# Performance work log

Hardware: AMD Instinct MI355X
Metric: run time of the kernel (lower is better)

The kernel has to match this reference:

```python
import jax, jax.numpy as jnp
import numpy as np

COEFF = 0.97  # de-emphasis coefficient (module init kwarg)


def setup_inputs() -> dict:
    key = jax.random.key(0)
    waveform = jax.random.normal(key, (32, 2, 480000), dtype=jnp.float32)
    return {"waveform": waveform}


def reference(waveform) -> jnp.ndarray:
    # y[n] = x[n] + COEFF * y[n-1] along the last axis.
    # Expressed as a first-order linear recurrence y_n = a_n*y_{n-1} + b_n
    # with a_n = COEFF (constant), b_n = x[n], solved with a log-depth
    # associative scan: (a1,b1) o (a2,b2) = (a1*a2, a2*b1 + b2).
    a = jnp.full_like(waveform, COEFF)

    def combine(left, right):
        a_l, b_l = left
        a_r, b_r = right
        return (a_l * a_r, a_r * b_l + b_r)

    _, y = jax.lax.associative_scan(combine, (a, waveform), axis=-1)
    return y
```

## Files before the change

kernel.cpp:

```cpp
#include <hip/hip_runtime.h>


#define COEFF 0.97f
#define ROW_LEN 480000
#define SEG 4
#define SPAN_W 256
#define HALO 512
#define P_HALO 2
#define P_OUT 15
#define P_TOT (P_OUT + P_HALO)
#define OUT_W (P_OUT * SPAN_W)
#define WPR (ROW_LEN / OUT_W)
#define BLOCK 256
#define WAVES (BLOCK / 64)
#define PF 8

typedef float v4f __attribute__((ext_vector_type(4)));

constexpr float fpow(float b, int n) {
    float r = 1.0f;
    for (int i = 0; i < n; ++i) r *= b;
    return r;
}
constexpr float S0 = fpow(COEFF, 4);
constexpr float S1 = fpow(COEFF, 8);
constexpr float S2 = fpow(COEFF, 16);
constexpr float S3 = fpow(COEFF, 32);
constexpr float S4 = fpow(COEFF, 64);
constexpr float S5 = fpow(COEFF, 128);
constexpr float CP = fpow(COEFF, SPAN_W);
constexpr float C1P = fpow(COEFF, 1);
constexpr float C2P = fpow(COEFF, 2);
constexpr float C3P = fpow(COEFF, 3);
constexpr float C4P = fpow(COEFF, 4);

__global__ __launch_bounds__(BLOCK, 8) void deemph_kernel(const float* __restrict__ x,
                                                          float* __restrict__ y) {
    const int lane = threadIdx.x & 63;
    const int wave = threadIdx.x >> 6;
    const int widx = blockIdx.x * WAVES + wave;
    if (widx >= WPR) return;
    const int row  = blockIdx.y;

    const float* __restrict__ xrow = x + (long long)row * ROW_LEN;
    float* __restrict__ yrow       = y + (long long)row * ROW_LEN;

    const int lbase = widx * OUT_W - HALO + 4 * lane;

    float Aex = 1.0f;
    if (lane & 1)  Aex *= S0;
    if (lane & 2)  Aex *= S1;
    if (lane & 4)  Aex *= S2;
    if (lane & 8)  Aex *= S3;
    if (lane & 16) Aex *= S4;
    if (lane & 32) Aex *= S5;

    v4f rb[PF];
    #pragma unroll
    for (int q = 0; q < PF; ++q) {
        const int e = lbase + q * SPAN_W;
        v4f v = {0.0f, 0.0f, 0.0f, 0.0f};
        if (e >= 0 && e < ROW_LEN) v = *(const v4f*)(xrow + e);
        rb[q] = v;
    }

    float c = 0.0f;
    #pragma unroll
    for (int p = 0; p < P_TOT; ++p) {
        v4f v = rb[p % PF];
        if (p + PF < P_TOT) {
            const int e2 = lbase + (p + PF) * SPAN_W;
            v4f nv = {0.0f, 0.0f, 0.0f, 0.0f};
            if (e2 >= 0 && e2 < ROW_LEN) nv = *(const v4f*)(xrow + e2);
            rb[p % PF] = nv;
        }

        const float l0 = v.x;
        const float l1 = fmaf(COEFF, l0, v.y);
        const float l2 = fmaf(COEFF, l1, v.z);
        const float l3 = fmaf(COEFF, l2, v.w);

        float Bv = l3, Bp;
        Bp = __shfl_up(Bv, 1);  if (lane >= 1)  Bv = fmaf(S0, Bp, Bv);
        Bp = __shfl_up(Bv, 2);  if (lane >= 2)  Bv = fmaf(S1, Bp, Bv);
        Bp = __shfl_up(Bv, 4);  if (lane >= 4)  Bv = fmaf(S2, Bp, Bv);
        Bp = __shfl_up(Bv, 8);  if (lane >= 8)  Bv = fmaf(S3, Bp, Bv);
        Bp = __shfl_up(Bv, 16); if (lane >= 16) Bv = fmaf(S4, Bp, Bv);
        Bp = __shfl_up(Bv, 32); if (lane >= 32) Bv = fmaf(S5, Bp, Bv);
        float Bex = __shfl_up(Bv, 1);
        if (lane == 0) Bex = 0.0f;
        const float B63 = __shfl(Bv, 63);

        const float Kt = fmaf(c, Aex, Bex);
        c = fmaf(c, CP, B63);

        if (p >= P_HALO) {
            const int e = lbase + p * SPAN_W;
            if (e < ROW_LEN) {
                v4f o;
                o.x = fmaf(Kt, C1P, l0);
                o.y = fmaf(Kt, C2P, l1);
                o.z = fmaf(Kt, C3P, l2);
                o.w = fmaf(Kt, C4P, l3);
                __builtin_nontemporal_store(o, (v4f*)(yrow + e));
            }
        }
    }
}

extern "C" void kernel_launch(void* const* d_in, const int* in_sizes, int n_in,
                              void* d_out, int out_size, void* d_ws, size_t ws_size,
                              hipStream_t stream) {
    (void)n_in; (void)d_ws; (void)ws_size; (void)out_size;
    const float* x = (const float*)d_in[0];
    float* y = (float*)d_out;
    const int n_rows = in_sizes[0] / ROW_LEN;
    dim3 grid((WPR + WAVES - 1) / WAVES, n_rows);
    deemph_kernel<<<grid, BLOCK, 0, stream>>>(x, y);
}
```

Measured before the change: 218.4 us.

## Batch all spans' loads and interleave shuffle scans across spans

All seventeen per-lane vector loads are issued up front, and the wave-level shuffle scan runs on all spans at once, so the seventeen independent shuffle chains interleave instead of running one dependent chain per span. The grid is flattened to 1D so waves pack across row boundaries, the halo-boundary checks are replaced by clamping with an explicit carry reset on the first window, and the broadcast of lane 63 uses readlane. Nontemporal stores become plain stores. Register pressure rises sharply, so launch bounds are relaxed to 4 blocks per SM, which may cost occupancy.

Measured after the change: 220.2 us. About the same (+0.8%).

```diff
diff --git a/kernel.cpp b/kernel.cpp
--- a/kernel.cpp
+++ b/kernel.cpp
@@ -3,7 +3,6 @@
 
 #define COEFF 0.97f
 #define ROW_LEN 480000
-#define SEG 4
 #define SPAN_W 256
 #define HALO 512
 #define P_HALO 2
@@ -13,7 +12,6 @@
 #define WPR (ROW_LEN / OUT_W)
 #define BLOCK 256
 #define WAVES (BLOCK / 64)
-#define PF 8
 
 typedef float v4f __attribute__((ext_vector_type(4)));
 
@@ -34,13 +32,29 @@
 constexpr float C3P = fpow(COEFF, 3);
 constexpr float C4P = fpow(COEFF, 4);
 
-__global__ __launch_bounds__(BLOCK, 8) void deemph_kernel(const float* __restrict__ x,
-                                                          float* __restrict__ y) {
+__device__ __forceinline__ float bcast63(float v) {
+    return __int_as_float(__builtin_amdgcn_readlane(__float_as_int(v), 63));
+}
+
+template <int D>
+__device__ __forceinline__ void scan_step(float (&Bv)[P_TOT], float F, int lane) {
+    float Bp[P_TOT];
+    #pragma unroll
+    for (int t = 0; t < P_TOT; ++t) Bp[t] = __shfl_up(Bv[t], D);
+    #pragma unroll
+    for (int t = 0; t < P_TOT; ++t)
+        if (lane >= D) Bv[t] = fmaf(F, Bp[t], Bv[t]);
+}
+
+__global__ __launch_bounds__(BLOCK, 4) void deemph_kernel(const float* __restrict__ x,
+                                                          float* __restrict__ y,
+                                                          int n_rows) {
     const int lane = threadIdx.x & 63;
     const int wave = threadIdx.x >> 6;
-    const int widx = blockIdx.x * WAVES + wave;
-    if (widx >= WPR) return;
-    const int row  = blockIdx.y;
+    const int gw   = blockIdx.x * WAVES + wave;
+    const int row  = gw / WPR;
+    const int widx = gw - row * WPR;
+    if (row >= n_rows) return;
 
     const float* __restrict__ xrow = x + (long long)row * ROW_LEN;
     float* __restrict__ yrow       = y + (long long)row * ROW_LEN;
@@ -55,55 +69,56 @@
     if (lane & 16) Aex *= S4;
     if (lane & 32) Aex *= S5;
 
-    v4f rb[PF];
+    v4f rb[P_TOT];
     #pragma unroll
-    for (int q = 0; q < PF; ++q) {
-        const int e = lbase + q * SPAN_W;
-        v4f v = {0.0f, 0.0f, 0.0f, 0.0f};
-        if (e >= 0 && e < ROW_LEN) v = *(const v4f*)(xrow + e);
-        rb[q] = v;
+    for (int t = 0; t < P_TOT; ++t) {
+        int e = lbase + t * SPAN_W;
+        e = e < 0 ? 0 : e;
+        rb[t] = *(const v4f*)(xrow + e);
     }
+    asm volatile("" ::: "memory");
+
+    #pragma unroll
+    for (int t = 0; t < P_TOT; ++t) {
+        rb[t].y = fmaf(COEFF, rb[t].x, rb[t].y);
+        rb[t].z = fmaf(COEFF, rb[t].y, rb[t].z);
+        rb[t].w = fmaf(COEFF, rb[t].z, rb[t].w);
+    }
+
+    float Bv[P_TOT];
+    #pragma unroll
+    for (int t = 0; t < P_TOT; ++t) Bv[t] = rb[t].w;
+    scan_step<1>(Bv, S0, lane);
+    scan_step<2>(Bv, S1, lane);
+    scan_step<4>(Bv, S2, lane);
+    scan_step<8>(Bv, S3, lane);
+    scan_step<16>(Bv, S4, lane);
+    scan_step<32>(Bv, S5, lane);
+
+    float Bex[P_TOT];
+    #pragma unroll
+    for (int t = 0; t < P_TOT; ++t) {
+        Bex[t] = __shfl_up(Bv[t], 1);
+        if (lane == 0) Bex[t] = 0.0f;
+    }
+    float B63[P_TOT];
+    #pragma unroll
+    for (int t = 0; t < P_TOT; ++t) B63[t] = bcast63(Bv[t]);
 
     float c = 0.0f;
     #pragma unroll
-    for (int p = 0; p < P_TOT; ++p) {
-        v4f v = rb[p % PF];
-        if (p + PF < P_TOT) {
-            const int e2 = lbase + (p + PF) * SPAN_W;
-            v4f nv = {0.0f, 0.0f, 0.0f, 0.0f};
-            if (e2 >= 0 && e2 < ROW_LEN) nv = *(const v4f*)(xrow + e2);
-            rb[p % PF] = nv;
-        }
-
-        const float l0 = v.x;
-        const float l1 = fmaf(COEFF, l0, v.y);
-        const float l2 = fmaf(COEFF, l1, v.z);
-        const float l3 = fmaf(COEFF, l2, v.w);
-
-        float Bv = l3, Bp;
-        Bp = __shfl_up(Bv, 1);  if (lane >= 1)  Bv = fmaf(S0, Bp, Bv);
-        Bp = __shfl_up(Bv, 2);  if (lane >= 2)  Bv = fmaf(S1, Bp, Bv);
-        Bp = __shfl_up(Bv, 4);  if (lane >= 4)  Bv = fmaf(S2, Bp, Bv);
-        Bp = __shfl_up(Bv, 8);  if (lane >= 8)  Bv = fmaf(S3, Bp, Bv);
-        Bp = __shfl_up(Bv, 16); if (lane >= 16) Bv = fmaf(S4, Bp, Bv);
-        Bp = __shfl_up(Bv, 32); if (lane >= 32) Bv = fmaf(S5, Bp, Bv);
-        float Bex = __shfl_up(Bv, 1);
-        if (lane == 0) Bex = 0.0f;
-        const float B63 = __shfl(Bv, 63);
-
-        const float Kt = fmaf(c, Aex, Bex);
-        c = fmaf(c, CP, B63);
-
-        if (p >= P_HALO) {
-            const int e = lbase + p * SPAN_W;
-            if (e < ROW_LEN) {
-                v4f o;
-                o.x = fmaf(Kt, C1P, l0);
-                o.y = fmaf(Kt, C2P, l1);
-                o.z = fmaf(Kt, C3P, l2);
-                o.w = fmaf(Kt, C4P, l3);
-                __builtin_nontemporal_store(o, (v4f*)(yrow + e));
-            }
+    for (int t = 0; t < P_TOT; ++t) {
+        if (t == P_HALO) c = (widx == 0) ? 0.0f : c;
+        const float Kt = fmaf(c, Aex, Bex[t]);
+        c = fmaf(c, CP, B63[t]);
+        if (t >= P_HALO) {
+            const int e = lbase + t * SPAN_W;
+            v4f o;
+            o.x = fmaf(Kt, C1P, rb[t].x);
+            o.y = fmaf(Kt, C2P, rb[t].y);
+            o.z = fmaf(Kt, C3P, rb[t].z);
+            o.w = fmaf(Kt, C4P, rb[t].w);
+            *(v4f*)(yrow + e) = o;
         }
     }
 }
@@ -115,6 +130,6 @@
     const float* x = (const float*)d_in[0];
     float* y = (float*)d_out;
     const int n_rows = in_sizes[0] / ROW_LEN;
-    dim3 grid((WPR + WAVES - 1) / WAVES, n_rows);
-    deemph_kernel<<<grid, BLOCK, 0, stream>>>(x, y);
+    const int nblocks = (WPR * n_rows + WAVES - 1) / WAVES;
+    deemph_kernel<<<dim3(nblocks), BLOCK, 0, stream>>>(x, y, n_rows);
 }
```

## Stream input through LDS with async global_load_lds ring and flattened grid

Applied to the files above, without the earlier changes.

Replaces the register prefetch buffer with a per-wave 6-slot LDS ring filled by global_load_lds DMA, with explicit vmcnt waits computed at compile time per pass. It also flattens the 2D grid into a 1D wave index so no waves sit idle at row ends, computes the exclusive prefix algebraically instead of with an extra shuffle, and uses readlane for the broadcast. Stores become normal rather than nontemporal, and bounds checks are dropped by clamping the halo address and zeroing the carry at row start. The goal is to cut VGPR pressure and load latency for a memory-bound scan, at the cost of fragile hand-counted waitcnt ordering and LDS usage per block.

Result: no change. 219.0 us (+0.3%).

```diff
diff --git a/kernel.cpp b/kernel.cpp
--- a/kernel.cpp
+++ b/kernel.cpp
@@ -3,7 +3,6 @@
 
 #define COEFF 0.97f
 #define ROW_LEN 480000
-#define SEG 4
 #define SPAN_W 256
 #define HALO 512
 #define P_HALO 2
@@ -13,7 +12,7 @@
 #define WPR (ROW_LEN / OUT_W)
 #define BLOCK 256
 #define WAVES (BLOCK / 64)
-#define PF 8
+#define RING 6
 
 typedef float v4f __attribute__((ext_vector_type(4)));
 
@@ -28,24 +27,107 @@
 constexpr float S3 = fpow(COEFF, 32);
 constexpr float S4 = fpow(COEFF, 64);
 constexpr float S5 = fpow(COEFF, 128);
-constexpr float CP = fpow(COEFF, SPAN_W);
+constexpr float CP  = fpow(COEFF, SPAN_W);
 constexpr float C1P = fpow(COEFF, 1);
 constexpr float C2P = fpow(COEFF, 2);
 constexpr float C3P = fpow(COEFF, 3);
 constexpr float C4P = fpow(COEFF, 4);
+constexpr float IC4 = 1.0f / fpow(COEFF, 4);
 
-__global__ __launch_bounds__(BLOCK, 8) void deemph_kernel(const float* __restrict__ x,
-                                                          float* __restrict__ y) {
+constexpr int wcnt(int P) {
+    const int hi  = (P + RING - 1 < P_TOT - 1) ? P + RING - 1 : P_TOT - 1;
+    const int dma = hi - P;
+    const int lo  = (P - RING > P_HALO) ? P - RING : P_HALO;
+    int st = P - lo;
+    if (st < 0) st = 0;
+    return dma + st;
+}
+
+__device__ __forceinline__ float bcast63(float v) {
+    return __int_as_float(__builtin_amdgcn_readlane(__float_as_int(v), 63));
+}
+
+__device__ __forceinline__ void issue_dma(const float* src, v4f* slot) {
+    __builtin_amdgcn_global_load_lds(
+        (const __attribute__((address_space(1))) void*)src,
+        (__attribute__((address_space(3))) void*)slot, 16, 0, 0);
+}
+
+struct WaveCtx {
+    const float* xrow;
+    float* yrow;
+    int   base0;
+    int   lane;
+    float Aex;
+    bool  row_start;
+};
+
+template <int P>
+__device__ __forceinline__ void run_pass(const WaveCtx& cx, v4f (*slots)[64],
+                                         float& c) {
+    if constexpr (P < P_TOT) {
+        asm volatile("s_waitcnt vmcnt(%0)" :: "i"(wcnt(P)) : "memory");
+
+        v4f v = slots[P % RING][cx.lane];
+        asm volatile("s_waitcnt lgkmcnt(0)" ::: "memory");
+
+        if constexpr (P + RING < P_TOT) {
+            const int be = cx.base0 + (P + RING) * SPAN_W;
+            issue_dma(cx.xrow + be + 4 * cx.lane, &slots[P % RING][0]);
+        }
+
+        const float l0 = v.x;
+        const float l1 = fmaf(COEFF, l0, v.y);
+        const float l2 = fmaf(COEFF, l1, v.z);
+        const float l3 = fmaf(COEFF, l2, v.w);
+
+        float Bv = l3, Bp;
+        Bp = __shfl_up(Bv, 1);  if (cx.lane >= 1)  Bv = fmaf(S0, Bp, Bv);
+        Bp = __shfl_up(Bv, 2);  if (cx.lane >= 2)  Bv = fmaf(S1, Bp, Bv);
+        Bp = __shfl_up(Bv, 4);  if (cx.lane >= 4)  Bv = fmaf(S2, Bp, Bv);
+        Bp = __shfl_up(Bv, 8);  if (cx.lane >= 8)  Bv = fmaf(S3, Bp, Bv);
+        Bp = __shfl_up(Bv, 16); if (cx.lane >= 16) Bv = fmaf(S4, Bp, Bv);
+        Bp = __shfl_up(Bv, 32); if (cx.lane >= 32) Bv = fmaf(S5, Bp, Bv);
+
+        const float Bex = (Bv - l3) * IC4;
+        const float B63 = bcast63(Bv);
+
+        float cc = c;
+        if constexpr (P == P_HALO) { if (cx.row_start) cc = 0.0f; }
+        const float Kt = fmaf(cc, cx.Aex, Bex);
+        c = fmaf(cc, CP, B63);
+
+        if constexpr (P >= P_HALO) {
+            const int e = cx.base0 + P * SPAN_W + 4 * cx.lane;
+            v4f o;
+            o.x = fmaf(Kt, C1P, l0);
+            o.y = fmaf(Kt, C2P, l1);
+            o.z = fmaf(Kt, C3P, l2);
+            o.w = fmaf(Kt, C4P, l3);
+            *(v4f*)(cx.yrow + e) = o;
+        }
+
+        run_pass<P + 1>(cx, slots, c);
+    }
+}
+
+__global__ __launch_bounds__(BLOCK, 6) void deemph_kernel(const float* __restrict__ x,
+                                                          float* __restrict__ y,
+                                                          int n_rows) {
+    __shared__ v4f lds[WAVES][RING][64];
     const int lane = threadIdx.x & 63;
     const int wave = threadIdx.x >> 6;
-    const int widx = blockIdx.x * WAVES + wave;
-    if (widx >= WPR) return;
-    const int row  = blockIdx.y;
+    const int gw   = blockIdx.x * WAVES + wave;
+    const int row  = gw / WPR;
+    const int widx = gw - row * WPR;
+    if (row >= n_rows) return;
 
-    const float* __restrict__ xrow = x + (long long)row * ROW_LEN;
-    float* __restrict__ yrow       = y + (long long)row * ROW_LEN;
-
-    const int lbase = widx * OUT_W - HALO + 4 * lane;
+    WaveCtx cx;
+    cx.xrow  = x + (long long)row * ROW_LEN;
+    cx.yrow  = y + (long long)row * ROW_LEN;
+    cx.base0 = widx * OUT_W - HALO;
+    cx.lane  = lane;
+    cx.row_start = (widx == 0);
 
     float Aex = 1.0f;
     if (lane & 1)  Aex *= S0;
@@ -54,58 +136,17 @@
     if (lane & 8)  Aex *= S3;
     if (lane & 16) Aex *= S4;
     if (lane & 32) Aex *= S5;
+    cx.Aex = Aex;
 
-    v4f rb[PF];
     #pragma unroll
-    for (int q = 0; q < PF; ++q) {
-        const int e = lbase + q * SPAN_W;
-        v4f v = {0.0f, 0.0f, 0.0f, 0.0f};
-        if (e >= 0 && e < ROW_LEN) v = *(const v4f*)(xrow + e);
-        rb[q] = v;
+    for (int q = 0; q < RING; ++q) {
+        int be = cx.base0 + q * SPAN_W;
+        be = be < 0 ? 0 : be;
+        issue_dma(cx.xrow + be + 4 * lane, &lds[wave][q][0]);
     }
 
     float c = 0.0f;
-    #pragma unroll
-    for (int p = 0; p < P_TOT; ++p) {
-        v4f v = rb[p % PF];
-        if (p + PF < P_TOT) {
-            const int e2 = lbase + (p + PF) * SPAN_W;
-            v4f nv = {0.0f, 0.0f, 0.0f, 0.0f};
-            if (e2 >= 0 && e2 < ROW_LEN) nv = *(const v4f*)(xrow + e2);
-            rb[p % PF] = nv;
-        }
-
-        const float l0 = v.x;
-        const float l1 = fmaf(COEFF, l0, v.y);
-        const float l2 = fmaf(COEFF, l1, v.z);
-        const float l3 = fmaf(COEFF, l2, v.w);
-
-        float Bv = l3, Bp;
-        Bp = __shfl_up(Bv, 1);  if (lane >= 1)  Bv = fmaf(S0, Bp, Bv);
-        Bp = __shfl_up(Bv, 2);  if (lane >= 2)  Bv = fmaf(S1, Bp, Bv);
-        Bp = __shfl_up(Bv, 4);  if (lane >= 4)  Bv = fmaf(S2, Bp, Bv);
-        Bp = __shfl_up(Bv, 8);  if (lane >= 8)  Bv = fmaf(S3, Bp, Bv);
-        Bp = __shfl_up(Bv, 16); if (lane >= 16) Bv = fmaf(S4, Bp, Bv);
-        Bp = __shfl_up(Bv, 32); if (lane >= 32) Bv = fmaf(S5, Bp, Bv);
-        float Bex = __shfl_up(Bv, 1);
-        if (lane == 0) Bex = 0.0f;
-        const float B63 = __shfl(Bv, 63);
-
-        const float Kt = fmaf(c, Aex, Bex);
-        c = fmaf(c, CP, B63);
-
-        if (p >= P_HALO) {
-            const int e = lbase + p * SPAN_W;
-            if (e < ROW_LEN) {
-                v4f o;
-                o.x = fmaf(Kt, C1P, l0);
-                o.y = fmaf(Kt, C2P, l1);
-                o.z = fmaf(Kt, C3P, l2);
-                o.w = fmaf(Kt, C4P, l3);
-                __builtin_nontemporal_store(o, (v4f*)(yrow + e));
-            }
-        }
-    }
+    run_pass<0>(cx, lds[wave], c);
 }
 
 extern "C" void kernel_launch(void* const* d_in, const int* in_sizes, int n_in,
@@ -115,6 +156,6 @@
     const float* x = (const float*)d_in[0];
     float* y = (float*)d_out;
     const int n_rows = in_sizes[0] / ROW_LEN;
-    dim3 grid((WPR + WAVES - 1) / WAVES, n_rows);
-    deemph_kernel<<<grid, BLOCK, 0, stream>>>(x, y);
+    const int nblocks = (WPR * n_rows + WAVES - 1) / WAVES;
+    deemph_kernel<<<dim3(nblocks), BLOCK, 0, stream>>>(x, y, n_rows);
 }
```

## Flatten grid, drop prefetch ring, derive exclusive scan algebraically, use readlane broadcast

Applied to the files above, without the earlier changes.

The 2D grid becomes a flat 1D wave index split into row and window, so blocks no longer idle at the end of each row. The explicit 8-deep register prefetch ring is replaced by a direct nontemporal load per step, with negative offsets clamped. A row-start flag zeroes the carry so the clamped halo data does not leak in. The exclusive prefix is computed algebraically as (Bv - l3)/c^4 instead of an extra shuffle, and lane 63 is broadcast with readlane. This trades explicit memory-level parallelism and a small amount of precision for fewer shuffles and registers, and it relies on the compiler to hoist the loads.

After: 209.3 us. 1.04x faster.

```diff
diff --git a/kernel.cpp b/kernel.cpp
--- a/kernel.cpp
+++ b/kernel.cpp
@@ -3,7 +3,6 @@
 
 #define COEFF 0.97f
 #define ROW_LEN 480000
-#define SEG 4
 #define SPAN_W 256
 #define HALO 512
 #define P_HALO 2
@@ -13,7 +12,6 @@
 #define WPR (ROW_LEN / OUT_W)
 #define BLOCK 256
 #define WAVES (BLOCK / 64)
-#define PF 8
 
 typedef float v4f __attribute__((ext_vector_type(4)));
 
@@ -28,24 +26,32 @@
 constexpr float S3 = fpow(COEFF, 32);
 constexpr float S4 = fpow(COEFF, 64);
 constexpr float S5 = fpow(COEFF, 128);
-constexpr float CP = fpow(COEFF, SPAN_W);
+constexpr float CP  = fpow(COEFF, SPAN_W);
 constexpr float C1P = fpow(COEFF, 1);
 constexpr float C2P = fpow(COEFF, 2);
 constexpr float C3P = fpow(COEFF, 3);
 constexpr float C4P = fpow(COEFF, 4);
+constexpr float IC4 = 1.0f / fpow(COEFF, 4);
+
+__device__ __forceinline__ float bcast63(float v) {
+    return __int_as_float(__builtin_amdgcn_readlane(__float_as_int(v), 63));
+}
 
 __global__ __launch_bounds__(BLOCK, 8) void deemph_kernel(const float* __restrict__ x,
-                                                          float* __restrict__ y) {
+                                                          float* __restrict__ y,
+                                                          int n_rows) {
     const int lane = threadIdx.x & 63;
     const int wave = threadIdx.x >> 6;
-    const int widx = blockIdx.x * WAVES + wave;
-    if (widx >= WPR) return;
-    const int row  = blockIdx.y;
+    const int gw   = blockIdx.x * WAVES + wave;
+    const int row  = gw / WPR;
+    const int widx = gw - row * WPR;
+    if (row >= n_rows) return;
 
     const float* __restrict__ xrow = x + (long long)row * ROW_LEN;
     float* __restrict__ yrow       = y + (long long)row * ROW_LEN;
 
     const int lbase = widx * OUT_W - HALO + 4 * lane;
+    const bool row_start = (widx == 0);
 
     float Aex = 1.0f;
     if (lane & 1)  Aex *= S0;
@@ -55,25 +61,12 @@
     if (lane & 16) Aex *= S4;
     if (lane & 32) Aex *= S5;
 
-    v4f rb[PF];
-    #pragma unroll
-    for (int q = 0; q < PF; ++q) {
-        const int e = lbase + q * SPAN_W;
-        v4f v = {0.0f, 0.0f, 0.0f, 0.0f};
-        if (e >= 0 && e < ROW_LEN) v = *(const v4f*)(xrow + e);
-        rb[q] = v;
-    }
-
     float c = 0.0f;
     #pragma unroll
     for (int p = 0; p < P_TOT; ++p) {
-        v4f v = rb[p % PF];
-        if (p + PF < P_TOT) {
-            const int e2 = lbase + (p + PF) * SPAN_W;
-            v4f nv = {0.0f, 0.0f, 0.0f, 0.0f};
-            if (e2 >= 0 && e2 < ROW_LEN) nv = *(const v4f*)(xrow + e2);
-            rb[p % PF] = nv;
-        }
+        int e = lbase + p * SPAN_W;
+        const int ec = e < 0 ? 0 : e;
+        const v4f v = __builtin_nontemporal_load((const v4f*)(xrow + ec));
 
         const float l0 = v.x;
         const float l1 = fmaf(COEFF, l0, v.y);
@@ -87,23 +80,22 @@
         Bp = __shfl_up(Bv, 8);  if (lane >= 8)  Bv = fmaf(S3, Bp, Bv);
         Bp = __shfl_up(Bv, 16); if (lane >= 16) Bv = fmaf(S4, Bp, Bv);
         Bp = __shfl_up(Bv, 32); if (lane >= 32) Bv = fmaf(S5, Bp, Bv);
-        float Bex = __shfl_up(Bv, 1);
-        if (lane == 0) Bex = 0.0f;
-        const float B63 = __shfl(Bv, 63);
 
-        const float Kt = fmaf(c, Aex, Bex);
-        c = fmaf(c, CP, B63);
+        const float Bex = (Bv - l3) * IC4;
+        const float B63 = bcast63(Bv);
+
+        float cc = c;
+        if (p == P_HALO && row_start) cc = 0.0f;
+        const float Kt = fmaf(cc, Aex, Bex);
+        c = fmaf(cc, CP, B63);
 
         if (p >= P_HALO) {
-            const int e = lbase + p * SPAN_W;
-            if (e < ROW_LEN) {
-                v4f o;
-                o.x = fmaf(Kt, C1P, l0);
-                o.y = fmaf(Kt, C2P, l1);
-                o.z = fmaf(Kt, C3P, l2);
-                o.w = fmaf(Kt, C4P, l3);
-                __builtin_nontemporal_store(o, (v4f*)(yrow + e));
-            }
+            v4f o;
+            o.x = fmaf(Kt, C1P, l0);
+            o.y = fmaf(Kt, C2P, l1);
+            o.z = fmaf(Kt, C3P, l2);
+            o.w = fmaf(Kt, C4P, l3);
+            __builtin_nontemporal_store(o, (v4f*)(yrow + e));
         }
     }
 }
@@ -115,6 +107,6 @@
     const float* x = (const float*)d_in[0];
     float* y = (float*)d_out;
     const int n_rows = in_sizes[0] / ROW_LEN;
-    dim3 grid((WPR + WAVES - 1) / WAVES, n_rows);
-    deemph_kernel<<<grid, BLOCK, 0, stream>>>(x, y);
+    const int nblocks = (WPR * n_rows + WAVES - 1) / WAVES;
+    deemph_kernel<<<dim3(nblocks), BLOCK, 0, stream>>>(x, y, n_rows);
 }
```
